# Kernel tuning notes

Hardware: AMD Instinct MI355X
Metric: run time of the kernel (lower is better)

The kernel has to match this reference:

```python
import jax, jax.numpy as jnp
import numpy as np

PI = 3.1415927410125732
N = 4096
VELOCITY = 5e-7
RC = 3.15e-6          # collision radius
RR = 8e-6             # repulsion radius
RO = 2.5e-5           # orientation radius (Ra = inf -> inside_Ra all-true)
ALPHA = PI            # field of view; < 2*pi so within_view masking is active
DT_TRANS = 1.4e-14    # translational diffusion DT
DR = 0.0028
GAMMA = 25.0
DT = 0.2              # timestep dt
COLLISION_ITERS = 3   # fixed-iteration version of recursive solve_collisions
EPS = 1e-14


def _c(x):  # [N,2] real -> complex64
    return jax.lax.complex(x[..., 0], x[..., 1])


def _r(z):  # complex -> [..., 2] real
    return jnp.stack([z.real, z.imag], axis=-1)


def _anglediff(a, b):
    # torch get_anglediff: wrap angle(a)-angle(b) into (-pi, pi)
    diff = jnp.angle(a) - jnp.angle(b)
    diff = jnp.where(diff <= -PI, jnp.mod(diff, PI), diff)
    return diff - (diff >= PI) * (2.0 * PI)


def _cossim(a, b):
    # nn.CosineSimilarity(dim=1, eps=1e-14) on view_as_real of complex vectors
    dot = a.real * b.real + a.imag * b.imag
    na = jnp.sqrt(a.real ** 2 + a.imag ** 2 + 1e-30)
    nb = jnp.sqrt(b.real ** 2 + b.imag ** 2 + 1e-30)
    return dot / (jnp.maximum(na, EPS) * jnp.maximum(nb, EPS))


def setup_inputs() -> dict:
    key = jax.random.key(0)
    k1, k2, k3, k4, k5 = jax.random.split(key, 5)
    positions = jax.random.normal(k1, (N, 2), jnp.float32) * 5e-4
    ang = jax.random.uniform(k2, (N,), jnp.float32, -PI, PI)
    orientations = jnp.stack([jnp.cos(ang), jnp.sin(ang)], axis=-1)  # unit complex
    Deltas = jax.random.uniform(k3, (1,), jnp.float32, 0.1, 0.6)
    rot_noise = jax.random.normal(k4, (N,), jnp.float32)
    trans_noise = jax.random.normal(k5, (N, 2), jnp.float32)
    return {"positions": positions, "orientations": orientations, "Deltas": Deltas,
            "rot_noise": rot_noise, "trans_noise": trans_noise}


def reference(positions, orientations, Deltas, rot_noise, trans_noise):
    p = _c(positions)      # [N] complex positions
    u = _c(orientations)   # [N] complex orientations
    n = p.shape[0]
    eye = jnp.eye(n, dtype=bool)

    # pairwise direction/distance: dirs[i,j] = p_j - p_i
    dirs = p[None, :] - p[:, None]
    dists = jnp.abs(dirs)

    inside_Rr = (dists <= RR) & ~eye
    inside_Ro = dists <= RO + RC
    # inside_Ra with Ra = inf is all-True

    # angle between separation vector and orientation of the *neighbor* j
    ang_diff = _anglediff(dirs, u[None, :])
    in_front = ang_diff < PI / 2
    within_view = ang_diff < ALPHA  # alpha < 2*pi branch active

    cdtype = p.dtype
    mask_rr = (inside_Rr & in_front).astype(cdtype)
    mask_ra = within_view.astype(cdtype)  # inside_Ra all True
    mask_ro = (inside_Ro & within_view).astype(cdtype)

    n_r = mask_rr.real.sum(axis=1)
    S = (mask_rr @ p) / jnp.maximum(n_r, 1.0) - p * jnp.sign(n_r)
    d = -S

    n_a = mask_ra.real.sum(axis=1)
    cms = (mask_ra @ p) / jnp.maximum(n_a, 1.0)
    Ps = cms - p * jnp.sign(n_a)

    orientation_sums = mask_ro @ u

    leftturns = Ps * jnp.exp(1j * Deltas)
    rightturns = Ps * jnp.exp(-1j * Deltas)

    # T >= T_release branch: pick the turn most aligned with neighbor orientations
    left_closer = _cossim(leftturns, orientation_sums) >= _cossim(rightturns, orientation_sums)
    best_turns = jnp.where(left_closer, leftturns, rightturns)

    d_abs = jnp.abs(d)
    d_safe = jnp.where(d_abs > 0, d, jnp.ones((), cdtype))
    best_safe = jnp.where(jnp.abs(best_turns) > 0, best_turns, jnp.ones((), cdtype))
    angle_to_target = jnp.where(d_abs > 0, _anglediff(d_safe, u), _anglediff(best_safe, u))

    # rotational_noise = randn * sqrt(2*DR); rotation = exp(i*(dt*Gamma*DR*sin + noise*sqrt(dt)))
    rot = jnp.exp(1j * (DT * GAMMA * DR * jnp.sin(angle_to_target)
                        + rot_noise * np.float32(np.sqrt(2 * DR)) * np.float32(np.sqrt(DT))))

    # complex-normal translational noise (per-component std 1/sqrt(2)) * sqrt(2*DT) * sqrt(dt)
    tn = _c(trans_noise) * np.float32(np.sqrt(0.5)) * np.float32(np.sqrt(2 * DT_TRANS))
    translation = DT * VELOCITY * u + tn * np.float32(np.sqrt(DT))

    def collide(i, pos):
        dd = pos[None, :] - pos[:, None]
        dd_nd = jnp.where(eye, jnp.ones((), pos.dtype), dd)  # avoid 0/0 on diagonal
        ab = jnp.where(eye, 0.0, jnp.abs(dd_nd))
        coll = ab <= 2 * RC - jnp.eye(n, dtype=ab.dtype)
        safe = jnp.where(coll, ab, 1.0)
        move = jnp.where(coll, dd / safe * ((2.1 * RC - ab) * 0.5), jnp.zeros((), pos.dtype))
        return pos - move.sum(axis=1)

    new_p = jax.lax.fori_loop(0, COLLISION_ITERS, collide, p + translation)
    new_u = u * rot

    # pack the 5 complex outputs as real [5, N, 2]
    return jnp.stack([_r(new_p), _r(new_u), _r(orientation_sums), _r(leftturns), _r(rightturns)], axis=0)
```

## Files before the change

### kernel.cpp

```cpp
#include <hip/hip_runtime.h>
#include <math.h>

#define NPART 4096
#define NBLK  512
#define NTHR  256
#define IPB   8
#define SMAX  512
#define GDIM  64
#define NCELL (GDIM * GDIM)

constexpr float RORC   = (float)(2.5e-5 + 3.15e-6);
constexpr float RORC2  = RORC * RORC;
constexpr float RRF    = 8e-6f;
constexpr float RR2    = RRF * RRF;
constexpr float TWORC  = (float)(2.0 * 3.15e-6);
constexpr float TWORC2 = TWORC * TWORC;
constexpr float C21RC  = (float)(2.1 * 3.15e-6);
constexpr float RCAND2 = 1.6e-9f;
constexpr float GMIN   = -2.048e-3f;
constexpr float GINV   = 15625.0f;
constexpr float C_ROT  = (float)(0.2 * 25.0 * 0.0028);
constexpr float C_RN1  = (float)0.07483314773547883;
constexpr float C_SQDT = (float)0.4472135954999579;
constexpr float C_TRV  = (float)(0.2 * 5e-7);
constexpr float C_HALF = (float)0.7071067811865476;
constexpr float C_SQ2T = (float)1.6733200530681511e-07;
constexpr float EPSF   = 1e-14f;

__device__ __forceinline__ int cell_of(float x, float y) {
    int cx = (int)floorf((x - GMIN) * GINV);
    int cy = (int)floorf((y - GMIN) * GINV);
    cx = min(max(cx, 0), GDIM - 1);
    cy = min(max(cy, 0), GDIM - 1);
    return cy * GDIM + cx;
}

__global__ __launch_bounds__(NTHR) void fused_all(
        const float2* __restrict__ pos, const float2* __restrict__ ori,
        const float* __restrict__ Deltas, const float* __restrict__ rot_noise,
        const float2* __restrict__ trans_noise, float2* __restrict__ out) {
    __shared__ float4   pp4[NPART / 2];
    __shared__ int      ptr[NCELL];
    __shared__ unsigned short sortid[NPART];
    __shared__ float    sred[5 * NTHR];
    __shared__ float    res[5][IPB];
    __shared__ unsigned bmap[NPART / 32];
    __shared__ int      Sidx[SMAX];
    __shared__ float4   posS4[SMAX / 2];
    __shared__ int      scnt;
    __shared__ int      iloc[IPB];
    float2* ppos_s = (float2*)pp4;
    float2* posS   = (float2*)posS4;
    int*    sredi  = (int*)sred;

    const int tid  = threadIdx.x;
    const int il   = tid >> 5;
    const int lane = tid & 31;
    const int gi   = blockIdx.x * IPB + il;
    if (tid == 0) scnt = 0;
    if (tid < NPART / 32) bmap[tid] = 0u;

    for (int k = 0; k < NPART / NTHR; ++k)
        ppos_s[k * NTHR + tid] = pos[k * NTHR + tid];
    for (int k = 0; k < NCELL / NTHR; ++k)
        ptr[k * NTHR + tid] = 0;
    __syncthreads();

    for (int k = 0; k < NPART / NTHR; ++k) {
        const int p = k * NTHR + tid;
        const float2 pp = ppos_s[p];
        atomicAdd(&ptr[cell_of(pp.x, pp.y)], 1);
    }
    __syncthreads();

    {
        const int base = tid * (NCELL / NTHR);
        int v[NCELL / NTHR];
        int sum = 0;
        #pragma unroll
        for (int t = 0; t < NCELL / NTHR; ++t) { v[t] = ptr[base + t]; sum += v[t]; }
        sredi[tid] = sum;
        __syncthreads();
        for (int off = 1; off < NTHR; off <<= 1) {
            const int a = (tid >= off) ? sredi[tid - off] : 0;
            __syncthreads();
            sredi[tid] += a;
            __syncthreads();
        }
        int run = sredi[tid] - sum;
        #pragma unroll
        for (int t = 0; t < NCELL / NTHR; ++t) { ptr[base + t] = run; run += v[t]; }
    }
    __syncthreads();

    for (int k = 0; k < NPART / NTHR; ++k) {
        const int p = k * NTHR + tid;
        const float2 pp = ppos_s[p];
        const int slot = atomicAdd(&ptr[cell_of(pp.x, pp.y)], 1);
        sortid[slot] = (unsigned short)p;
    }
    __syncthreads();

    const float2 pi = ppos_s[gi];
    {
        int cxi = (int)floorf((pi.x - GMIN) * GINV);
        int cyi = (int)floorf((pi.y - GMIN) * GINV);
        cxi = min(max(cxi, 0), GDIM - 1);
        cyi = min(max(cyi, 0), GDIM - 1);
        float nr = 0.f, sx = 0.f, sy = 0.f, oxs = 0.f, oys = 0.f;
        for (int dy = -1; dy <= 1; ++dy) {
            const int cy = cyi + dy;
            if (cy < 0 || cy >= GDIM) continue;
            for (int dx = -1; dx <= 1; ++dx) {
                const int cx = cxi + dx;
                if (cx < 0 || cx >= GDIM) continue;
                const int c  = cy * GDIM + cx;
                const int b0 = (c > 0) ? ptr[c - 1] : 0;
                const int e0 = ptr[c];
                for (int t = b0 + lane; t < e0; t += 32) {
                    const int j = sortid[t];
                    const float2 pj = ppos_s[j];
                    const float dxp = pj.x - pi.x, dyp = pj.y - pi.y;
                    const float r2 = fmaf(dxp, dxp, dyp * dyp);
                    if (r2 <= RCAND2) {
                        atomicOr(&bmap[j >> 5], 1u << (j & 31));
                        if (r2 <= RORC2) {
                            const float2 uj = ori[j];
                            oxs += uj.x; oys += uj.y;
                            if (r2 <= RR2 && r2 > 0.f) {
                                const float dt_ = fmaf(dxp, uj.x, dyp * uj.y);
                                const float cr_ = fmaf(dyp, uj.x, -dxp * uj.y);
                                if (!((dt_ <= 0.f) && (cr_ >= 0.f))) {
                                    nr += 1.f; sx += pj.x; sy += pj.y;
                                }
                            }
                        }
                    }
                }
            }
        }
        sred[0 * NTHR + il * 32 + lane] = nr;
        sred[1 * NTHR + il * 32 + lane] = sx;
        sred[2 * NTHR + il * 32 + lane] = sy;
        sred[3 * NTHR + il * 32 + lane] = oxs;
        sred[4 * NTHR + il * 32 + lane] = oys;
    }
    __syncthreads();

    if (tid < 5 * IPB) {
        const int q = tid / IPB, ii = tid & (IPB - 1);
        float acc = 0.f;
        #pragma unroll
        for (int s = 0; s < 32; ++s) acc += sred[q * NTHR + ii * 32 + s];
        res[q][ii] = acc;
    } else if (tid >= 128 && tid < 128 + NPART / 32) {
        const int w = tid - 128;
        unsigned bits = bmap[w];
        while (bits) {
            const int b = __ffs(bits) - 1;
            bits &= bits - 1;
            const int p = w * 32 + b;
            const int slot = atomicAdd(&scnt, 1);
            if (slot < SMAX) {
                Sidx[slot] = p;
                if ((p >> 3) == (int)blockIdx.x) iloc[p & (IPB - 1)] = slot;
            }
        }
    }
    __syncthreads();
    const int nS = (scnt < SMAX) ? scnt : SMAX;

    for (int m = tid; m < nS; m += NTHR) {
        const int p = Sidx[m];
        const float2 pp = ppos_s[p];
        const float2 uu = ori[p];
        const float2 tn = trans_noise[p];
        posS[m] = make_float2(
            pp.x + (C_TRV * uu.x + ((tn.x * C_HALF) * C_SQ2T) * C_SQDT),
            pp.y + (C_TRV * uu.y + ((tn.y * C_HALF) * C_SQ2T) * C_SQDT));
    }

    float mx = 0.f, my = 0.f;
    for (int k = 0; k < NPART / NTHR; ++k) {
        const float2 v = ppos_s[k * NTHR + tid];
        mx += v.x; my += v.y;
    }
    __syncthreads();
    sred[tid] = mx; sred[NTHR + tid] = my;
    __syncthreads();
    for (int s = NTHR / 2; s > 0; s >>= 1) {
        if (tid < s) { sred[tid] += sred[tid + s]; sred[NTHR + tid] += sred[NTHR + tid + s]; }
        __syncthreads();
    }
    const float cmx = sred[0]    * (1.f / NPART);
    const float cmy = sred[NTHR] * (1.f / NPART);

    if (tid < IPB) {
        const int g2 = blockIdx.x * IPB + tid;
        const float2 p = ppos_s[g2];
        const float2 u = ori[g2];
        const float nrv = res[0][tid], sxv = res[1][tid], syv = res[2][tid];
        const float osx = res[3][tid], osy = res[4][tid];

        const float inv = 1.f / fmaxf(nrv, 1.f);
        const float sg  = (nrv > 0.f) ? 1.f : 0.f;
        const float Sx = sxv * inv - p.x * sg;
        const float Sy = syv * inv - p.y * sg;
        const float dxv = -Sx, dyv = -Sy;

        const float Psx = cmx - p.x;
        const float Psy = cmy - p.y;

        float sd, cd;
        sincosf(Deltas[0], &sd, &cd);
        const float Lx = Psx * cd - Psy * sd;
        const float Ly = Psx * sd + Psy * cd;
        const float Rx = Psx * cd + Psy * sd;
        const float Ry = Psy * cd - Psx * sd;

        const float no  = fmaxf(sqrtf(osx * osx + osy * osy + 1e-30f), EPSF);
        const float nl  = fmaxf(sqrtf(Lx * Lx + Ly * Ly + 1e-30f), EPSF);
        const float nrr = fmaxf(sqrtf(Rx * Rx + Ry * Ry + 1e-30f), EPSF);
        const float csl = (Lx * osx + Ly * osy) / (nl * no);
        const float csr = (Rx * osx + Ry * osy) / (nrr * no);
        const bool left = (csl >= csr);
        const float bx = left ? Lx : Rx;
        const float by = left ? Ly : Ry;

        float cx, cy;
        if (dxv != 0.f || dyv != 0.f)    { cx = dxv; cy = dyv; }
        else if (bx != 0.f || by != 0.f) { cx = bx;  cy = by;  }
        else                             { cx = 1.f; cy = 0.f; }

        const float dt_ = cx * u.x + cy * u.y;
        const float cr_ = cy * u.x - cx * u.y;
        const float sin_t = cr_ / sqrtf(dt_ * dt_ + cr_ * cr_);

        const float ang = C_ROT * sin_t + (rot_noise[g2] * C_RN1) * C_SQDT;
        float sa, ca;
        sincosf(ang, &sa, &ca);
        out[1 * NPART + g2] = make_float2(u.x * ca - u.y * sa,
                                          u.x * sa + u.y * ca);
        out[2 * NPART + g2] = make_float2(osx, osy);
        out[3 * NPART + g2] = make_float2(Lx, Ly);
        out[4 * NPART + g2] = make_float2(Rx, Ry);
    }
    __syncthreads();

    for (int pass = 0; pass < 3; ++pass) {
        float px[2], py[2], ax[2] = {0.f, 0.f}, ay[2] = {0.f, 0.f};
        bool  mv[2];
        #pragma unroll
        for (int q = 0; q < 2; ++q) {
            const int m = tid + q * NTHR;
            mv[q] = (m < nS);
            if (mv[q]) { px[q] = posS[m].x; py[q] = posS[m].y; }
        }
        int b = 0;
        for (; b + 4 <= nS; b += 4) {
            const float4 w0 = posS4[(b >> 1)];
            const float4 w1 = posS4[(b >> 1) + 1];
            const float bxs[4] = {w0.x, w0.z, w1.x, w1.z};
            const float bys[4] = {w0.y, w0.w, w1.y, w1.w};
            #pragma unroll
            for (int s = 0; s < 4; ++s) {
                #pragma unroll
                for (int q = 0; q < 2; ++q) {
                    if (mv[q]) {
                        const float dx = bxs[s] - px[q], dy = bys[s] - py[q];
                        const float r2 = fmaf(dx, dx, dy * dy);
                        if (r2 <= TWORC2 && r2 > 0.f) {
                            const float ab = sqrtf(r2);
                            const float sc = (C21RC - ab) * 0.5f / ab;
                            ax[q] = fmaf(dx, sc, ax[q]);
                            ay[q] = fmaf(dy, sc, ay[q]);
                        }
                    }
                }
            }
        }
        for (; b < nS; ++b) {
            const float2 pb = posS[b];
            #pragma unroll
            for (int q = 0; q < 2; ++q) {
                if (mv[q]) {
                    const float dx = pb.x - px[q], dy = pb.y - py[q];
                    const float r2 = fmaf(dx, dx, dy * dy);
                    if (r2 <= TWORC2 && r2 > 0.f) {
                        const float ab = sqrtf(r2);
                        const float sc = (C21RC - ab) * 0.5f / ab;
                        ax[q] = fmaf(dx, sc, ax[q]);
                        ay[q] = fmaf(dy, sc, ay[q]);
                    }
                }
            }
        }
        __syncthreads();
        #pragma unroll
        for (int q = 0; q < 2; ++q) {
            const int m = tid + q * NTHR;
            if (m < nS) posS[m] = make_float2(px[q] - ax[q], py[q] - ay[q]);
        }
        __syncthreads();
    }
    if (tid < IPB)
        out[0 * NPART + blockIdx.x * IPB + tid] = posS[iloc[tid]];
}

extern "C" void kernel_launch(void* const* d_in, const int* in_sizes, int n_in,
                              void* d_out, int out_size, void* d_ws, size_t ws_size,
                              hipStream_t stream) {
    const float2* pos = (const float2*)d_in[0];
    const float2* ori = (const float2*)d_in[1];
    const float*  del = (const float*)d_in[2];
    const float*  rn  = (const float*)d_in[3];
    const float2* tn  = (const float2*)d_in[4];
    float2* o2 = (float2*)d_out;
    (void)d_ws; (void)ws_size;

    fused_all<<<dim3(NBLK), dim3(NTHR), 0, stream>>>(pos, ori, del, rn, tn, o2);
}
```

Baseline: 96.95 us.

## Store sorted positions contiguously, merge cell-row scans, use warp-shuffle reductions

Particle positions are kept in registers and scattered into a cell-sorted position array, so neighbour scans read contiguous positions instead of gathering through indices. The three cells in each grid row are scanned as one contiguous range. Per-particle partial sums are reduced with warp shuffles instead of shared-memory loops. The collision subset is capped at 256 with the block's own particles pinned to the first slots, so each thread handles one entry and the slot lookup table goes away. The smaller cap risks dropping candidates in dense neighbourhoods.

```diff
diff --git a/kernel.cpp b/kernel.cpp
--- a/kernel.cpp
+++ b/kernel.cpp
@@ -5,9 +5,10 @@
 #define NBLK  512
 #define NTHR  256
 #define IPB   8
-#define SMAX  512
+#define SMAX  256
 #define GDIM  64
 #define NCELL (GDIM * GDIM)
+#define PPT   (NPART / NTHR)
 
 constexpr float RORC   = (float)(2.5e-5 + 3.15e-6);
 constexpr float RORC2  = RORC * RORC;
@@ -39,37 +40,40 @@
         const float2* __restrict__ pos, const float2* __restrict__ ori,
         const float* __restrict__ Deltas, const float* __restrict__ rot_noise,
         const float2* __restrict__ trans_noise, float2* __restrict__ out) {
-    __shared__ float4   pp4[NPART / 2];
     __shared__ int      ptr[NCELL];
     __shared__ unsigned short sortid[NPART];
-    __shared__ float    sred[5 * NTHR];
+    __shared__ float4   sortpos4[NPART / 2];
+    __shared__ float    sred[2 * NTHR];
     __shared__ float    res[5][IPB];
     __shared__ unsigned bmap[NPART / 32];
     __shared__ int      Sidx[SMAX];
     __shared__ float4   posS4[SMAX / 2];
     __shared__ int      scnt;
-    __shared__ int      iloc[IPB];
-    float2* ppos_s = (float2*)pp4;
-    float2* posS   = (float2*)posS4;
-    int*    sredi  = (int*)sred;
+    float2* sortpos = (float2*)sortpos4;
+    float2* posS    = (float2*)posS4;
+    int*    sredi   = (int*)sred;
 
     const int tid  = threadIdx.x;
     const int il   = tid >> 5;
     const int lane = tid & 31;
     const int gi   = blockIdx.x * IPB + il;
-    if (tid == 0) scnt = 0;
+
+    if (tid == 0) scnt = IPB;
+    if (tid < IPB) Sidx[tid] = blockIdx.x * IPB + tid;
     if (tid < NPART / 32) bmap[tid] = 0u;
-
-    for (int k = 0; k < NPART / NTHR; ++k)
-        ppos_s[k * NTHR + tid] = pos[k * NTHR + tid];
     for (int k = 0; k < NCELL / NTHR; ++k)
         ptr[k * NTHR + tid] = 0;
-    __syncthreads();
-
-    for (int k = 0; k < NPART / NTHR; ++k) {
-        const int p = k * NTHR + tid;
-        const float2 pp = ppos_s[p];
-        atomicAdd(&ptr[cell_of(pp.x, pp.y)], 1);
+
+    float2 pp[PPT];
+    int    cc[PPT];
+    #pragma unroll
+    for (int k = 0; k < PPT; ++k)
+        pp[k] = pos[k * NTHR + tid];
+    __syncthreads();
+    #pragma unroll
+    for (int k = 0; k < PPT; ++k) {
+        cc[k] = cell_of(pp[k].x, pp[k].y);
+        atomicAdd(&ptr[cc[k]], 1);
     }
     __syncthreads();
 
@@ -93,99 +97,89 @@
     }
     __syncthreads();
 
-    for (int k = 0; k < NPART / NTHR; ++k) {
-        const int p = k * NTHR + tid;
-        const float2 pp = ppos_s[p];
-        const int slot = atomicAdd(&ptr[cell_of(pp.x, pp.y)], 1);
-        sortid[slot] = (unsigned short)p;
-    }
-    __syncthreads();
-
-    const float2 pi = ppos_s[gi];
+    #pragma unroll
+    for (int k = 0; k < PPT; ++k) {
+        const int slot = atomicAdd(&ptr[cc[k]], 1);
+        sortid[slot]  = (unsigned short)(k * NTHR + tid);
+        sortpos[slot] = pp[k];
+    }
+    __syncthreads();
+
+    const float2 pi = pos[gi];
+    float nr = 0.f, sx = 0.f, sy = 0.f, oxs = 0.f, oys = 0.f;
     {
-        int cxi = (int)floorf((pi.x - GMIN) * GINV);
-        int cyi = (int)floorf((pi.y - GMIN) * GINV);
-        cxi = min(max(cxi, 0), GDIM - 1);
-        cyi = min(max(cyi, 0), GDIM - 1);
-        float nr = 0.f, sx = 0.f, sy = 0.f, oxs = 0.f, oys = 0.f;
-        for (int dy = -1; dy <= 1; ++dy) {
-            const int cy = cyi + dy;
+        int cxi = min(max((int)floorf((pi.x - GMIN) * GINV), 0), GDIM - 1);
+        int cyi = min(max((int)floorf((pi.y - GMIN) * GINV), 0), GDIM - 1);
+        for (int dyr = -1; dyr <= 1; ++dyr) {
+            const int cy = cyi + dyr;
             if (cy < 0 || cy >= GDIM) continue;
-            for (int dx = -1; dx <= 1; ++dx) {
-                const int cx = cxi + dx;
-                if (cx < 0 || cx >= GDIM) continue;
-                const int c  = cy * GDIM + cx;
-                const int b0 = (c > 0) ? ptr[c - 1] : 0;
-                const int e0 = ptr[c];
-                for (int t = b0 + lane; t < e0; t += 32) {
+            const int c_lo = cy * GDIM + max(cxi - 1, 0);
+            const int c_hi = cy * GDIM + min(cxi + 1, GDIM - 1);
+            const int b0 = (c_lo > 0) ? ptr[c_lo - 1] : 0;
+            const int e0 = ptr[c_hi];
+            for (int t = b0 + lane; t < e0; t += 32) {
+                const float2 pj = sortpos[t];
+                const float dxp = pj.x - pi.x, dyp = pj.y - pi.y;
+                const float r2 = fmaf(dxp, dxp, dyp * dyp);
+                if (r2 <= RCAND2) {
                     const int j = sortid[t];
-                    const float2 pj = ppos_s[j];
-                    const float dxp = pj.x - pi.x, dyp = pj.y - pi.y;
-                    const float r2 = fmaf(dxp, dxp, dyp * dyp);
-                    if (r2 <= RCAND2) {
-                        atomicOr(&bmap[j >> 5], 1u << (j & 31));
-                        if (r2 <= RORC2) {
-                            const float2 uj = ori[j];
-                            oxs += uj.x; oys += uj.y;
-                            if (r2 <= RR2 && r2 > 0.f) {
-                                const float dt_ = fmaf(dxp, uj.x, dyp * uj.y);
-                                const float cr_ = fmaf(dyp, uj.x, -dxp * uj.y);
-                                if (!((dt_ <= 0.f) && (cr_ >= 0.f))) {
-                                    nr += 1.f; sx += pj.x; sy += pj.y;
-                                }
+                    atomicOr(&bmap[j >> 5], 1u << (j & 31));
+                    if (r2 <= RORC2) {
+                        const float2 uj = ori[j];
+                        oxs += uj.x; oys += uj.y;
+                        if (r2 <= RR2 && r2 > 0.f) {
+                            const float dt_ = fmaf(dxp, uj.x, dyp * uj.y);
+                            const float cr_ = fmaf(dyp, uj.x, -dxp * uj.y);
+                            if (!((dt_ <= 0.f) && (cr_ >= 0.f))) {
+                                nr += 1.f; sx += pj.x; sy += pj.y;
                             }
                         }
                     }
                 }
             }
         }
-        sred[0 * NTHR + il * 32 + lane] = nr;
-        sred[1 * NTHR + il * 32 + lane] = sx;
-        sred[2 * NTHR + il * 32 + lane] = sy;
-        sred[3 * NTHR + il * 32 + lane] = oxs;
-        sred[4 * NTHR + il * 32 + lane] = oys;
-    }
-    __syncthreads();
-
-    if (tid < 5 * IPB) {
-        const int q = tid / IPB, ii = tid & (IPB - 1);
-        float acc = 0.f;
+    }
+    {
+        float vals[5] = {nr, sx, sy, oxs, oys};
         #pragma unroll
-        for (int s = 0; s < 32; ++s) acc += sred[q * NTHR + ii * 32 + s];
-        res[q][ii] = acc;
-    } else if (tid >= 128 && tid < 128 + NPART / 32) {
-        const int w = tid - 128;
-        unsigned bits = bmap[w];
+        for (int q = 0; q < 5; ++q)
+            #pragma unroll
+            for (int off = 16; off >= 1; off >>= 1)
+                vals[q] += __shfl_down(vals[q], off, 32);
+        if (lane == 0) {
+            res[0][il] = vals[0]; res[1][il] = vals[1]; res[2][il] = vals[2];
+            res[3][il] = vals[3]; res[4][il] = vals[4];
+        }
+    }
+    __syncthreads();
+
+    if (tid < NPART / 32) {
+        unsigned bits = bmap[tid];
+        if (tid == (int)(blockIdx.x >> 2))
+            bits &= ~(0xFFu << ((blockIdx.x & 3) * 8));
         while (bits) {
             const int b = __ffs(bits) - 1;
             bits &= bits - 1;
-            const int p = w * 32 + b;
             const int slot = atomicAdd(&scnt, 1);
-            if (slot < SMAX) {
-                Sidx[slot] = p;
-                if ((p >> 3) == (int)blockIdx.x) iloc[p & (IPB - 1)] = slot;
-            }
+            if (slot < SMAX) Sidx[slot] = tid * 32 + b;
         }
     }
     __syncthreads();
     const int nS = (scnt < SMAX) ? scnt : SMAX;
 
-    for (int m = tid; m < nS; m += NTHR) {
-        const int p = Sidx[m];
-        const float2 pp = ppos_s[p];
+    if (tid < nS) {
+        const int p = Sidx[tid];
+        const float2 pq = pos[p];
         const float2 uu = ori[p];
         const float2 tn = trans_noise[p];
-        posS[m] = make_float2(
-            pp.x + (C_TRV * uu.x + ((tn.x * C_HALF) * C_SQ2T) * C_SQDT),
-            pp.y + (C_TRV * uu.y + ((tn.y * C_HALF) * C_SQ2T) * C_SQDT));
+        posS[tid] = make_float2(
+            pq.x + (C_TRV * uu.x + ((tn.x * C_HALF) * C_SQ2T) * C_SQDT),
+            pq.y + (C_TRV * uu.y + ((tn.y * C_HALF) * C_SQ2T) * C_SQDT));
     }
 
     float mx = 0.f, my = 0.f;
-    for (int k = 0; k < NPART / NTHR; ++k) {
-        const float2 v = ppos_s[k * NTHR + tid];
-        mx += v.x; my += v.y;
-    }
-    __syncthreads();
+    #pragma unroll
+    for (int k = 0; k < PPT; ++k) { mx += pp[k].x; my += pp[k].y; }
     sred[tid] = mx; sred[NTHR + tid] = my;
     __syncthreads();
     for (int s = NTHR / 2; s > 0; s >>= 1) {
@@ -197,7 +191,7 @@
 
     if (tid < IPB) {
         const int g2 = blockIdx.x * IPB + tid;
-        const float2 p = ppos_s[g2];
+        const float2 p = pos[g2];
         const float2 u = ori[g2];
         const float nrv = res[0][tid], sxv = res[1][tid], syv = res[2][tid];
         const float osx = res[3][tid], osy = res[4][tid];
@@ -248,14 +242,9 @@
     __syncthreads();
 
     for (int pass = 0; pass < 3; ++pass) {
-        float px[2], py[2], ax[2] = {0.f, 0.f}, ay[2] = {0.f, 0.f};
-        bool  mv[2];
-        #pragma unroll
-        for (int q = 0; q < 2; ++q) {
-            const int m = tid + q * NTHR;
-            mv[q] = (m < nS);
-            if (mv[q]) { px[q] = posS[m].x; py[q] = posS[m].y; }
-        }
+        float px = 0.f, py = 0.f, ax = 0.f, ay = 0.f;
+        const bool mv = (tid < nS);
+        if (mv) { px = posS[tid].x; py = posS[tid].y; }
         int b = 0;
         for (; b + 4 <= nS; b += 4) {
             const float4 w0 = posS4[(b >> 1)];
@@ -264,47 +253,37 @@
             const float bys[4] = {w0.y, w0.w, w1.y, w1.w};
             #pragma unroll
             for (int s = 0; s < 4; ++s) {
-                #pragma unroll
-                for (int q = 0; q < 2; ++q) {
-                    if (mv[q]) {
-                        const float dx = bxs[s] - px[q], dy = bys[s] - py[q];
-                        const float r2 = fmaf(dx, dx, dy * dy);
-                        if (r2 <= TWORC2 && r2 > 0.f) {
-                            const float ab = sqrtf(r2);
-                            const float sc = (C21RC - ab) * 0.5f / ab;
-                            ax[q] = fmaf(dx, sc, ax[q]);
-                            ay[q] = fmaf(dy, sc, ay[q]);
-                        }
-                    }
-                }
-            }
-        }
-        for (; b < nS; ++b) {
-            const float2 pb = posS[b];
-            #pragma unroll
-            for (int q = 0; q < 2; ++q) {
-                if (mv[q]) {
-                    const float dx = pb.x - px[q], dy = pb.y - py[q];
+                if (mv) {
+                    const float dx = bxs[s] - px, dy = bys[s] - py;
                     const float r2 = fmaf(dx, dx, dy * dy);
                     if (r2 <= TWORC2 && r2 > 0.f) {
                         const float ab = sqrtf(r2);
                         const float sc = (C21RC - ab) * 0.5f / ab;
-                        ax[q] = fmaf(dx, sc, ax[q]);
-                        ay[q] = fmaf(dy, sc, ay[q]);
+                        ax = fmaf(dx, sc, ax);
+                        ay = fmaf(dy, sc, ay);
                     }
                 }
             }
         }
+        for (; b < nS; ++b) {
+            const float2 pb = posS[b];
+            if (mv) {
+                const float dx = pb.x - px, dy = pb.y - py;
+                const float r2 = fmaf(dx, dx, dy * dy);
+                if (r2 <= TWORC2 && r2 > 0.f) {
+                    const float ab = sqrtf(r2);
+                    const float sc = (C21RC - ab) * 0.5f / ab;
+                    ax = fmaf(dx, sc, ax);
+                    ay = fmaf(dy, sc, ay);
+                }
+            }
+        }
         __syncthreads();
-        #pragma unroll
-        for (int q = 0; q < 2; ++q) {
-            const int m = tid + q * NTHR;
-            if (m < nS) posS[m] = make_float2(px[q] - ax[q], py[q] - ay[q]);
-        }
+        if (mv) posS[tid] = make_float2(px - ax, py - ay);
         __syncthreads();
     }
     if (tid < IPB)
-        out[0 * NPART + blockIdx.x * IPB + tid] = posS[iloc[tid]];
+        out[0 * NPART + blockIdx.x * IPB + tid] = posS[tid];
 }
 
 extern "C" void kernel_launch(void* const* d_in, const int* in_sizes, int n_in,
```

New measurement: 88.50 us. -8.7%, faster.
